# Kernel tuning notes

Measured on AMD Instinct MI355X. Metric: run time of the kernel, lower is better.

Reference implementation:

```python
import jax, jax.numpy as jnp
import numpy as np

N = 150000      # active voxels
C = 64          # head input channels
KK = 9          # 3x3 kernel offsets
H = W = 700     # BEV feature map
BN_EPS = 1e-5
HEADS = [("heatmap", 3), ("center", 2), ("center_z", 1), ("dim", 3), ("rot", 2)]


def _build_neighbor_table(seed=0):
    """Submanifold 3x3 neighbor indices for N active voxels on an HxW grid.
    Entry -1 means the neighbor site is inactive (contributes zero)."""
    rng = np.random.default_rng(seed)
    flat = rng.choice(H * W, size=N, replace=False)
    ys, xs = flat // W, flat % W
    lut = np.full(H * W, -1, np.int64)
    lut[flat] = np.arange(N)
    nbr = np.full((N, KK), -1, np.int64)
    k = 0
    for dy in (-1, 0, 1):
        for dx in (-1, 0, 1):
            ny, nx = ys + dy, xs + dx
            valid = (ny >= 0) & (ny < H) & (nx >= 0) & (nx < W)
            nf = np.where(valid, ny * W + nx, 0)
            nbr[:, k] = np.where(valid, lut[nf], -1)
            k += 1
    return nbr


def setup_inputs() -> dict:
    key = jax.random.key(0)
    ks = jax.random.split(key, 2 + 2 * len(HEADS))
    inp = {
        "features": jax.random.normal(ks[0], (N, C), jnp.float32),
        "nbr_idx": jnp.asarray(_build_neighbor_table(), jnp.int32),
        # one 3x3 subm conv per head, stacked: [n_heads, 9, C_in, C_out]
        "W3": jax.random.normal(ks[1], (len(HEADS), KK, C, C), jnp.float32) * 0.05,
        "gamma": jnp.ones((len(HEADS), C), jnp.float32),
        "beta": jnp.zeros((len(HEADS), C), jnp.float32),
    }
    for i, (name, oc) in enumerate(HEADS):
        inp[f"W1_{name}"] = jax.random.normal(ks[2 + i], (C, oc), jnp.float32) * 0.001
        if name == "heatmap":
            inp[f"b1_{name}"] = jnp.full((oc,), -float(np.log((1 - 0.01) / 0.01)), jnp.float32)
        else:
            inp[f"b1_{name}"] = jnp.zeros((oc,), jnp.float32)
    return inp


def _forward(features, nbr_idx, W3, gamma, beta, W1s, b1s):
    valid = nbr_idx >= 0                                  # [N, 9]
    idx = jnp.where(valid, nbr_idx, 0)
    # gather active-neighbor features; missing neighbors -> zero (subm conv)
    gathered = features[idx] * valid[..., None].astype(features.dtype)  # [N, 9, C]
    # all heads share the same input sparse tensor -> batched gather-GEMM
    h = jnp.einsum('nkc,hkco->hno', gathered, W3)         # [n_heads, N, C]
    # BatchNorm1d (training-mode batch stats, biased var) + ReLU
    mean = h.mean(axis=1, keepdims=True)
    var = ((h - mean) ** 2).mean(axis=1, keepdims=True)
    hn = (h - mean) * jax.lax.rsqrt(var + BN_EPS)
    hn = jax.nn.relu(hn * gamma[:, None, :] + beta[:, None, :])
    # per-head 1x1 subm conv == linear on active features
    return tuple(hn[i] @ W1s[i] + b1s[i] for i in range(len(HEADS)))


def reference(features, nbr_idx, W3, gamma, beta,
              W1_heatmap, b1_heatmap, W1_center, b1_center,
              W1_center_z, b1_center_z, W1_dim, b1_dim, W1_rot, b1_rot):
    W1s = [W1_heatmap, W1_center, W1_center_z, W1_dim, W1_rot]
    b1s = [b1_heatmap, b1_center, b1_center_z, b1_dim, b1_rot]
    return _forward(features, nbr_idx, W3, gamma, beta, W1s, b1s)
```

## Files before the change

kernel.cpp:

```cpp
#include <hip/hip_runtime.h>

#define NVOX 150000
#define BM 128
#define MTILES 1172
#define SROW 150016
#define NCOL 320

typedef __attribute__((ext_vector_type(8))) short bf16x8;
typedef __attribute__((ext_vector_type(4))) float f32x4;

__device__ __forceinline__ unsigned short f2bf(float f) {
    unsigned u = __builtin_bit_cast(unsigned, f);
    u += 0x7fffu + ((u >> 16) & 1u);
    return (unsigned short)(u >> 16);
}

__device__ __forceinline__ void gld16(const void* g, void* l) {
    __builtin_amdgcn_global_load_lds(
        (const __attribute__((address_space(1))) unsigned int*)g,
        (__attribute__((address_space(3))) unsigned int*)l, 16, 0, 0);
}

__global__ void prep_feat(const float* __restrict__ src, unsigned short* __restrict__ dst) {
    int i = blockIdx.x * 256 + threadIdx.x;
    if (i < NVOX * 64) dst[i] = f2bf(src[i]);
    else if (i < NVOX * 64 + 64) dst[i] = 0;
}

__global__ void prep_w3(const float* __restrict__ w3, unsigned short* __restrict__ bt,
                        float* __restrict__ stats) {
    int i = blockIdx.x * 256 + threadIdx.x;
    int h = i / 36864;
    int rem = i - h * 36864;
    int kk = rem >> 12;
    int c = (rem >> 6) & 63;
    int o = rem & 63;
    bt[(size_t)(((h * 9 + kk) * 8) + (c >> 3)) * 512 + o * 8 + (c & 7)] = f2bf(w3[i]);
    if (i < 2 * NCOL) stats[i] = 0.f;
}

__global__ __launch_bounds__(256, 4)
void gemm_kernel(const unsigned short* __restrict__ featB,
                 const unsigned short* __restrict__ Bt2,
                 const int* __restrict__ nbr,
                 unsigned short* __restrict__ hbuf,
                 float* __restrict__ stats) {
    __shared__ __align__(16) char smem[30208];
    constexpr int SB_OFF = 16384;
    constexpr int IDX_OFF = 24576;
    constexpr int SRED_OFF = 29184;

    int bid = blockIdx.x;
    int r = bid & 7, q = bid >> 3;
    int ntile = q % 5;
    int mtile = (q / 5) * 8 + r;
    if (mtile >= MTILES) return;
    int m0 = mtile * BM;
    int n0 = ntile * 64;

    int tid = threadIdx.x;
    int w = tid >> 6, lane = tid & 63;
    int quad = lane >> 4, m16 = lane & 15;

    for (int lin = tid; lin < BM * 9; lin += 256) {
        int row = lin / 9, kkq = lin - row * 9;
        int v = -1;
        if (m0 + row < NVOX) v = nbr[(size_t)(m0 + row) * 9 + kkq];
        *(int*)(smem + IDX_OFF + (kkq * BM + row) * 4) = ((v < 0) ? NVOX : v) * 128;
    }
    __syncthreads();

    f32x4 acc[4][2];
#pragma unroll
    for (int mt = 0; mt < 4; ++mt)
#pragma unroll
        for (int nt = 0; nt < 2; ++nt)
            acc[mt][nt] = (f32x4){0.f, 0.f, 0.f, 0.f};

    const char* fb = (const char*)featB;
    const char* bsrc = (const char*)Bt2 + (size_t)ntile * 73728;
    char* sA = smem;
    char* sB = smem + SB_OFF;

    int mrow = (w >> 1) * 64;
    int ncol = (w & 1) * 32;

    for (int kk = 0; kk < 9; ++kk) {
        int off0 = *(const int*)(smem + IDX_OFF + (kk * BM + lane) * 4);
        int off1 = *(const int*)(smem + IDX_OFF + (kk * BM + 64 + lane) * 4);
        int c16a = w * 2, c16b = w * 2 + 1;
        gld16(fb + off0 + c16a * 16, sA + c16a * 2048);
        gld16(fb + off1 + c16a * 16, sA + c16a * 2048 + 1024);
        gld16(fb + off0 + c16b * 16, sA + c16b * 2048);
        gld16(fb + off1 + c16b * 16, sA + c16b * 2048 + 1024);
        gld16(bsrc + (kk * 8 + c16a) * 1024 + lane * 16, sB + c16a * 1024);
        gld16(bsrc + (kk * 8 + c16b) * 1024 + lane * 16, sB + c16b * 1024);
        __syncthreads();
        bf16x8 af[2][4], bfr[2][2];
#pragma unroll
        for (int ks = 0; ks < 2; ++ks) {
#pragma unroll
            for (int mt = 0; mt < 4; ++mt)
                af[ks][mt] = *(const bf16x8*)(sA + (ks * 4 + quad) * 2048 +
                                              (mrow + mt * 16 + m16) * 16);
#pragma unroll
            for (int nt = 0; nt < 2; ++nt)
                bfr[ks][nt] = *(const bf16x8*)(sB + (ks * 4 + quad) * 1024 +
                                               (ncol + nt * 16 + m16) * 16);
        }
#pragma unroll
        for (int ks = 0; ks < 2; ++ks)
#pragma unroll
            for (int mt = 0; mt < 4; ++mt)
#pragma unroll
                for (int nt = 0; nt < 2; ++nt)
                    acc[mt][nt] = __builtin_amdgcn_mfma_f32_16x16x32_bf16(
                        af[ks][mt], bfr[ks][nt], acc[mt][nt], 0, 0, 0);
        __syncthreads();
    }

#pragma unroll
    for (int mt = 0; mt < 4; ++mt) {
#pragma unroll
        for (int nt = 0; nt < 2; ++nt) {
            int col = ncol + nt * 16 + m16;
            int row = mrow + mt * 16 + quad * 4;
            f32x4 v = acc[mt][nt];
            unsigned lo = (unsigned)f2bf(v.x) | ((unsigned)f2bf(v.y) << 16);
            unsigned hi = (unsigned)f2bf(v.z) | ((unsigned)f2bf(v.w) << 16);
            uint2 pk; pk.x = lo; pk.y = hi;
            *(uint2*)(smem + col * 272 + row * 2) = pk;
        }
    }
    __syncthreads();
#pragma unroll
    for (int it = 0; it < 8; ++it) {
        int col = it * 8 + (tid >> 5);
        int l32 = tid & 31;
        uint2 v = *(const uint2*)(smem + col * 272 + l32 * 8);
        *(uint2*)(hbuf + (size_t)(n0 + col) * SROW + m0 + l32 * 4) = v;
    }

    float s[2], ss[2];
#pragma unroll
    for (int nt = 0; nt < 2; ++nt) {
        float a = 0.f, b = 0.f;
#pragma unroll
        for (int mt = 0; mt < 4; ++mt) {
            f32x4 v = acc[mt][nt];
            a += v.x + v.y + v.z + v.w;
            b += v.x * v.x + v.y * v.y + v.z * v.z + v.w * v.w;
        }
        s[nt] = a; ss[nt] = b;
        s[nt] += __shfl_xor(s[nt], 16); s[nt] += __shfl_xor(s[nt], 32);
        ss[nt] += __shfl_xor(ss[nt], 16); ss[nt] += __shfl_xor(ss[nt], 32);
    }
    if (quad == 0) {
#pragma unroll
        for (int nt = 0; nt < 2; ++nt) {
            float* p = (float*)(smem + SRED_OFF + ((w * 2 + nt) * 16 + m16) * 8);
            p[0] = s[nt]; p[1] = ss[nt];
        }
    }
    __syncthreads();
    if (tid < 64) {
        int col = tid;
        int half = col >> 5, nt = (col >> 4) & 1, mc = col & 15;
        const float* p0 = (const float*)(smem + SRED_OFF + ((half * 2 + nt) * 16 + mc) * 8);
        const float* p1 = (const float*)(smem + SRED_OFF + (((2 + half) * 2 + nt) * 16 + mc) * 8);
        atomicAdd(&stats[n0 + col], p0[0] + p1[0]);
        atomicAdd(&stats[NCOL + n0 + col], p0[1] + p1[1]);
    }
}

__global__ void head_kernel(const unsigned short* __restrict__ hbuf,
                            const float* __restrict__ stats,
                            const float* __restrict__ gamma, const float* __restrict__ beta,
                            const float* __restrict__ W1_0, const float* __restrict__ W1_1,
                            const float* __restrict__ W1_2, const float* __restrict__ W1_3,
                            const float* __restrict__ W1_4,
                            const float* __restrict__ b1_0, const float* __restrict__ b1_1,
                            const float* __restrict__ b1_2, const float* __restrict__ b1_3,
                            const float* __restrict__ b1_4,
                            float* __restrict__ out) {
    __shared__ float sScale[NCOL], sShift[NCOL], sW1[NCOL * 3], sB1[16];
    int tid = threadIdx.x;
    for (int c = tid; c < NCOL; c += 256) {
        float mean = stats[c] * (1.f / (float)NVOX);
        float var = stats[NCOL + c] * (1.f / (float)NVOX) - mean * mean;
        float inv = rsqrtf(var + 1e-5f);
        float sc = inv * gamma[c];
        sScale[c] = sc;
        sShift[c] = beta[c] - mean * sc;
    }
    for (int i = tid; i < 192; i += 256) { int cc = i / 3, jj = i - cc * 3; sW1[0 * 192 + i] = W1_0[cc * 3 + jj]; }
    for (int i = tid; i < 192; i += 256) { int cc = i / 3, jj = i - cc * 3; sW1[1 * 192 + i] = (jj < 2) ? W1_1[cc * 2 + jj] : 0.f; }
    for (int i = tid; i < 192; i += 256) { int cc = i / 3, jj = i - cc * 3; sW1[2 * 192 + i] = (jj < 1) ? W1_2[cc] : 0.f; }
    for (int i = tid; i < 192; i += 256) { int cc = i / 3, jj = i - cc * 3; sW1[3 * 192 + i] = W1_3[cc * 3 + jj]; }
    for (int i = tid; i < 192; i += 256) { int cc = i / 3, jj = i - cc * 3; sW1[4 * 192 + i] = (jj < 2) ? W1_4[cc * 2 + jj] : 0.f; }
    if (tid == 0) {
        sB1[0] = b1_0[0]; sB1[1] = b1_0[1]; sB1[2] = b1_0[2];
        sB1[3] = b1_1[0]; sB1[4] = b1_1[1]; sB1[5] = 0.f;
        sB1[6] = b1_2[0]; sB1[7] = 0.f;    sB1[8] = 0.f;
        sB1[9] = b1_3[0]; sB1[10] = b1_3[1]; sB1[11] = b1_3[2];
        sB1[12] = b1_4[0]; sB1[13] = b1_4[1]; sB1[14] = 0.f;
    }
    __syncthreads();
    int n = 2 * (blockIdx.x * 256 + tid);
    if (n >= NVOX) return;
    const unsigned short* hp = hbuf + n;
#pragma unroll
    for (int h = 0; h < 5; ++h) {
        float x0 = sB1[h * 3 + 0], x1 = sB1[h * 3 + 1], x2 = sB1[h * 3 + 2];
        float y0 = x0, y1 = x1, y2 = x2;
#pragma unroll 8
        for (int cc = 0; cc < 64; ++cc) {
            int c = h * 64 + cc;
            unsigned raw = *(const unsigned*)(hp + (size_t)c * SROW);
            float v0 = __builtin_bit_cast(float, raw << 16);
            float v1 = __builtin_bit_cast(float, raw & 0xffff0000u);
            float sc = sScale[c], sh = sShift[c];
            v0 = fmaxf(v0 * sc + sh, 0.f);
            v1 = fmaxf(v1 * sc + sh, 0.f);
            float w0 = sW1[c * 3 + 0], w1 = sW1[c * 3 + 1], w2 = sW1[c * 3 + 2];
            x0 += v0 * w0; x1 += v0 * w1; x2 += v0 * w2;
            y0 += v1 * w0; y1 += v1 * w1; y2 += v1 * w2;
        }
        if (h == 0) {
            out[n * 3 + 0] = x0; out[n * 3 + 1] = x1; out[n * 3 + 2] = x2;
            out[(n + 1) * 3 + 0] = y0; out[(n + 1) * 3 + 1] = y1; out[(n + 1) * 3 + 2] = y2;
        } else if (h == 1) {
            out[450000 + n * 2 + 0] = x0; out[450000 + n * 2 + 1] = x1;
            out[450000 + (n + 1) * 2 + 0] = y0; out[450000 + (n + 1) * 2 + 1] = y1;
        } else if (h == 2) {
            out[750000 + n] = x0; out[750000 + n + 1] = y0;
        } else if (h == 3) {
            out[900000 + n * 3 + 0] = x0; out[900000 + n * 3 + 1] = x1; out[900000 + n * 3 + 2] = x2;
            out[900000 + (n + 1) * 3 + 0] = y0; out[900000 + (n + 1) * 3 + 1] = y1; out[900000 + (n + 1) * 3 + 2] = y2;
        } else {
            out[1350000 + n * 2 + 0] = x0; out[1350000 + n * 2 + 1] = x1;
            out[1350000 + (n + 1) * 2 + 0] = y0; out[1350000 + (n + 1) * 2 + 1] = y1;
        }
    }
}

extern "C" void kernel_launch(void* const* d_in, const int* in_sizes, int n_in,
                              void* d_out, int out_size, void* d_ws, size_t ws_size,
                              hipStream_t stream) {
    const float* features = (const float*)d_in[0];
    const int* nbr        = (const int*)d_in[1];
    const float* w3       = (const float*)d_in[2];
    const float* gamma    = (const float*)d_in[3];
    const float* beta     = (const float*)d_in[4];
    const float* W1_0 = (const float*)d_in[5];  const float* b1_0 = (const float*)d_in[6];
    const float* W1_1 = (const float*)d_in[7];  const float* b1_1 = (const float*)d_in[8];
    const float* W1_2 = (const float*)d_in[9];  const float* b1_2 = (const float*)d_in[10];
    const float* W1_3 = (const float*)d_in[11]; const float* b1_3 = (const float*)d_in[12];
    const float* W1_4 = (const float*)d_in[13]; const float* b1_4 = (const float*)d_in[14];
    float* out = (float*)d_out;

    char* ws = (char*)d_ws;
    unsigned short* featB = (unsigned short*)ws;
    unsigned short* Bt2   = (unsigned short*)(ws + 19200128);
    float* stats          = (float*)(ws + 19568768);
    unsigned short* hbuf  = (unsigned short*)(ws + 19571328);

    prep_feat<<<(NVOX * 64 + 64 + 255) / 256, 256, 0, stream>>>(features, featB);
    prep_w3<<<184320 / 256, 256, 0, stream>>>(w3, Bt2, stats);
    gemm_kernel<<<8 * 5 * 147, 256, 0, stream>>>(featB, Bt2, nbr, hbuf, stats);
    head_kernel<<<(NVOX / 2 + 255) / 256, 256, 0, stream>>>(hbuf, stats, gamma, beta,
        W1_0, W1_1, W1_2, W1_3, W1_4, b1_0, b1_1, b1_2, b1_3, b1_4, out);
}
```

Baseline: 230.6 us.

## Enlarge GEMM M-tile, load weights to registers, vectorize prep, split head by head

The gather-GEMM tile grows to 256 rows, with each wave computing 64 rows by all 64 columns. Weight fragments now load straight from global into registers from a new row-major Bt layout instead of being staged through LDS, and occupancy bounds drop to 3 waves per SIMD. prep_feat now converts four floats per thread, and head_kernel spreads the five heads across separate threads for more parallelism. Together these aim to reuse each gathered A tile across more columns and to cut per-element overhead, at the cost of higher register pressure and more LDS per block.

```diff
diff --git a/kernel.cpp b/kernel.cpp
--- a/kernel.cpp
+++ b/kernel.cpp
@@ -1,13 +1,14 @@
 #include <hip/hip_runtime.h>
 
 #define NVOX 150000
-#define BM 128
-#define MTILES 1172
+#define BM 256
+#define MTILES 586
 #define SROW 150016
 #define NCOL 320
 
 typedef __attribute__((ext_vector_type(8))) short bf16x8;
 typedef __attribute__((ext_vector_type(4))) float f32x4;
+typedef __attribute__((ext_vector_type(4))) unsigned short us4;
 
 __device__ __forceinline__ unsigned short f2bf(float f) {
     unsigned u = __builtin_bit_cast(unsigned, f);
@@ -23,8 +24,14 @@
 
 __global__ void prep_feat(const float* __restrict__ src, unsigned short* __restrict__ dst) {
     int i = blockIdx.x * 256 + threadIdx.x;
-    if (i < NVOX * 64) dst[i] = f2bf(src[i]);
-    else if (i < NVOX * 64 + 64) dst[i] = 0;
+    if (i < NVOX * 16) {
+        const float4 v = *(const float4*)(src + (size_t)i * 4);
+        us4 o; o.x = f2bf(v.x); o.y = f2bf(v.y); o.z = f2bf(v.z); o.w = f2bf(v.w);
+        *(us4*)(dst + (size_t)i * 4) = o;
+    } else if (i < NVOX * 16 + 16) {
+        us4 z; z.x = 0; z.y = 0; z.z = 0; z.w = 0;
+        *(us4*)(dst + (size_t)i * 4) = z;
+    }
 }
 
 __global__ void prep_w3(const float* __restrict__ w3, unsigned short* __restrict__ bt,
@@ -35,20 +42,19 @@
     int kk = rem >> 12;
     int c = (rem >> 6) & 63;
     int o = rem & 63;
-    bt[(size_t)(((h * 9 + kk) * 8) + (c >> 3)) * 512 + o * 8 + (c & 7)] = f2bf(w3[i]);
+    bt[(size_t)(h * 64 + o) * 576 + kk * 64 + c] = f2bf(w3[i]);
     if (i < 2 * NCOL) stats[i] = 0.f;
 }
 
-__global__ __launch_bounds__(256, 4)
+__global__ __launch_bounds__(256, 3)
 void gemm_kernel(const unsigned short* __restrict__ featB,
-                 const unsigned short* __restrict__ Bt2,
+                 const unsigned short* __restrict__ Bt,
                  const int* __restrict__ nbr,
                  unsigned short* __restrict__ hbuf,
                  float* __restrict__ stats) {
-    __shared__ __align__(16) char smem[30208];
-    constexpr int SB_OFF = 16384;
-    constexpr int IDX_OFF = 24576;
-    constexpr int SRED_OFF = 29184;
+    __shared__ __align__(16) char smem[44032];
+    constexpr int IDX_OFF = 32768;
+    constexpr int SRED_OFF = 41984;
 
     int bid = blockIdx.x;
     int r = bid & 7, q = bid >> 3;
@@ -62,74 +68,77 @@
     int w = tid >> 6, lane = tid & 63;
     int quad = lane >> 4, m16 = lane & 15;
 
-    for (int lin = tid; lin < BM * 9; lin += 256) {
-        int row = lin / 9, kkq = lin - row * 9;
-        int v = -1;
-        if (m0 + row < NVOX) v = nbr[(size_t)(m0 + row) * 9 + kkq];
-        *(int*)(smem + IDX_OFF + (kkq * BM + row) * 4) = ((v < 0) ? NVOX : v) * 128;
-    }
-    __syncthreads();
-
-    f32x4 acc[4][2];
+    for (int lin = tid; lin < 2304; lin += 256) {
+        int kkq = lin >> 8, row = lin & 255;
+        int v = (m0 + row < NVOX) ? nbr[(size_t)(m0 + row) * 9 + kkq] : -1;
+        *(int*)(smem + IDX_OFF + lin * 4) = ((v < 0) ? NVOX : v) * 128;
+    }
+    __syncthreads();
+
+    f32x4 acc[4][4];
 #pragma unroll
     for (int mt = 0; mt < 4; ++mt)
 #pragma unroll
-        for (int nt = 0; nt < 2; ++nt)
+        for (int nt = 0; nt < 4; ++nt)
             acc[mt][nt] = (f32x4){0.f, 0.f, 0.f, 0.f};
 
     const char* fb = (const char*)featB;
-    const char* bsrc = (const char*)Bt2 + (size_t)ntile * 73728;
+    const unsigned short* bb[4];
+#pragma unroll
+    for (int nt = 0; nt < 4; ++nt)
+        bb[nt] = Bt + (size_t)(n0 + nt * 16 + m16) * 576 + quad * 8;
+
     char* sA = smem;
-    char* sB = smem + SB_OFF;
-
-    int mrow = (w >> 1) * 64;
-    int ncol = (w & 1) * 32;
 
     for (int kk = 0; kk < 9; ++kk) {
-        int off0 = *(const int*)(smem + IDX_OFF + (kk * BM + lane) * 4);
-        int off1 = *(const int*)(smem + IDX_OFF + (kk * BM + 64 + lane) * 4);
-        int c16a = w * 2, c16b = w * 2 + 1;
-        gld16(fb + off0 + c16a * 16, sA + c16a * 2048);
-        gld16(fb + off1 + c16a * 16, sA + c16a * 2048 + 1024);
-        gld16(fb + off0 + c16b * 16, sA + c16b * 2048);
-        gld16(fb + off1 + c16b * 16, sA + c16b * 2048 + 1024);
-        gld16(bsrc + (kk * 8 + c16a) * 1024 + lane * 16, sB + c16a * 1024);
-        gld16(bsrc + (kk * 8 + c16b) * 1024 + lane * 16, sB + c16b * 1024);
+        int off[4];
+#pragma unroll
+        for (int rg = 0; rg < 4; ++rg)
+            off[rg] = *(const int*)(smem + IDX_OFF + (kk * 256 + rg * 64 + lane) * 4);
+#pragma unroll
+        for (int cc = 0; cc < 2; ++cc) {
+            int c16 = w * 2 + cc;
+#pragma unroll
+            for (int rg = 0; rg < 4; ++rg)
+                gld16(fb + off[rg] + c16 * 16, sA + c16 * 4096 + rg * 1024 + lane * 16);
+        }
+        bf16x8 bfr[2][4];
+#pragma unroll
+        for (int ks = 0; ks < 2; ++ks)
+#pragma unroll
+            for (int nt = 0; nt < 4; ++nt)
+                bfr[ks][nt] = *(const bf16x8*)(bb[nt] + kk * 64 + ks * 32);
         __syncthreads();
-        bf16x8 af[2][4], bfr[2][2];
-#pragma unroll
-        for (int ks = 0; ks < 2; ++ks) {
+        bf16x8 af[2][4];
+#pragma unroll
+        for (int ks = 0; ks < 2; ++ks)
 #pragma unroll
             for (int mt = 0; mt < 4; ++mt)
-                af[ks][mt] = *(const bf16x8*)(sA + (ks * 4 + quad) * 2048 +
-                                              (mrow + mt * 16 + m16) * 16);
-#pragma unroll
-            for (int nt = 0; nt < 2; ++nt)
-                bfr[ks][nt] = *(const bf16x8*)(sB + (ks * 4 + quad) * 1024 +
-                                               (ncol + nt * 16 + m16) * 16);
-        }
+                af[ks][mt] = *(const bf16x8*)(sA + (ks * 4 + quad) * 4096 +
+                                              (w * 64 + mt * 16 + m16) * 16);
 #pragma unroll
         for (int ks = 0; ks < 2; ++ks)
 #pragma unroll
             for (int mt = 0; mt < 4; ++mt)
 #pragma unroll
-                for (int nt = 0; nt < 2; ++nt)
+                for (int nt = 0; nt < 4; ++nt)
                     acc[mt][nt] = __builtin_amdgcn_mfma_f32_16x16x32_bf16(
                         af[ks][mt], bfr[ks][nt], acc[mt][nt], 0, 0, 0);
         __syncthreads();
     }
 
+    unsigned short* sOut = (unsigned short*)smem;
 #pragma unroll
     for (int mt = 0; mt < 4; ++mt) {
 #pragma unroll
-        for (int nt = 0; nt < 2; ++nt) {
-            int col = ncol + nt * 16 + m16;
-            int row = mrow + mt * 16 + quad * 4;
+        for (int nt = 0; nt < 4; ++nt) {
+            int col = nt * 16 + m16;
+            int row = w * 64 + mt * 16 + quad * 4;
             f32x4 v = acc[mt][nt];
             unsigned lo = (unsigned)f2bf(v.x) | ((unsigned)f2bf(v.y) << 16);
             unsigned hi = (unsigned)f2bf(v.z) | ((unsigned)f2bf(v.w) << 16);
             uint2 pk; pk.x = lo; pk.y = hi;
-            *(uint2*)(smem + col * 272 + row * 2) = pk;
+            *(uint2*)(sOut + col * 264 + row) = pk;
         }
     }
     __syncthreads();
@@ -137,13 +146,13 @@
     for (int it = 0; it < 8; ++it) {
         int col = it * 8 + (tid >> 5);
         int l32 = tid & 31;
-        uint2 v = *(const uint2*)(smem + col * 272 + l32 * 8);
-        *(uint2*)(hbuf + (size_t)(n0 + col) * SROW + m0 + l32 * 4) = v;
-    }
-
-    float s[2], ss[2];
-#pragma unroll
-    for (int nt = 0; nt < 2; ++nt) {
+        uint4 v = *(const uint4*)(sOut + col * 264 + l32 * 8);
+        *(uint4*)(hbuf + (size_t)(n0 + col) * SROW + m0 + l32 * 8) = v;
+    }
+
+    float s[4], ss[4];
+#pragma unroll
+    for (int nt = 0; nt < 4; ++nt) {
         float a = 0.f, b = 0.f;
 #pragma unroll
         for (int mt = 0; mt < 4; ++mt) {
@@ -155,21 +164,25 @@
         s[nt] += __shfl_xor(s[nt], 16); s[nt] += __shfl_xor(s[nt], 32);
         ss[nt] += __shfl_xor(ss[nt], 16); ss[nt] += __shfl_xor(ss[nt], 32);
     }
+    float* sRed = (float*)(smem + SRED_OFF);
     if (quad == 0) {
 #pragma unroll
-        for (int nt = 0; nt < 2; ++nt) {
-            float* p = (float*)(smem + SRED_OFF + ((w * 2 + nt) * 16 + m16) * 8);
-            p[0] = s[nt]; p[1] = ss[nt];
+        for (int nt = 0; nt < 4; ++nt) {
+            sRed[((w * 4 + nt) * 16 + m16) * 2 + 0] = s[nt];
+            sRed[((w * 4 + nt) * 16 + m16) * 2 + 1] = ss[nt];
         }
     }
     __syncthreads();
     if (tid < 64) {
-        int col = tid;
-        int half = col >> 5, nt = (col >> 4) & 1, mc = col & 15;
-        const float* p0 = (const float*)(smem + SRED_OFF + ((half * 2 + nt) * 16 + mc) * 8);
-        const float* p1 = (const float*)(smem + SRED_OFF + (((2 + half) * 2 + nt) * 16 + mc) * 8);
-        atomicAdd(&stats[n0 + col], p0[0] + p1[0]);
-        atomicAdd(&stats[NCOL + n0 + col], p0[1] + p1[1]);
+        int nt = tid >> 4, c = tid & 15;
+        float a = 0.f, b = 0.f;
+#pragma unroll
+        for (int ww = 0; ww < 4; ++ww) {
+            a += sRed[((ww * 4 + nt) * 16 + c) * 2 + 0];
+            b += sRed[((ww * 4 + nt) * 16 + c) * 2 + 1];
+        }
+        atomicAdd(&stats[n0 + tid], a);
+        atomicAdd(&stats[NCOL + n0 + tid], b);
     }
 }
 
@@ -206,41 +219,42 @@
         sB1[12] = b1_4[0]; sB1[13] = b1_4[1]; sB1[14] = 0.f;
     }
     __syncthreads();
-    int n = 2 * (blockIdx.x * 256 + tid);
-    if (n >= NVOX) return;
+    int lin = blockIdx.x * 256 + tid;
+    int h = lin / 75008;
+    int rp = lin - h * 75008;
+    if (rp >= 75000) return;
+    int n = rp * 2;
     const unsigned short* hp = hbuf + n;
-#pragma unroll
-    for (int h = 0; h < 5; ++h) {
-        float x0 = sB1[h * 3 + 0], x1 = sB1[h * 3 + 1], x2 = sB1[h * 3 + 2];
-        float y0 = x0, y1 = x1, y2 = x2;
+    float x0 = sB1[h * 3 + 0], x1 = sB1[h * 3 + 1], x2 = sB1[h * 3 + 2];
+    float y0 = x0, y1 = x1, y2 = x2;
+    int cbase = h * 64;
 #pragma unroll 8
-        for (int cc = 0; cc < 64; ++cc) {
-            int c = h * 64 + cc;
-            unsigned raw = *(const unsigned*)(hp + (size_t)c * SROW);
-            float v0 = __builtin_bit_cast(float, raw << 16);
-            float v1 = __builtin_bit_cast(float, raw & 0xffff0000u);
-            float sc = sScale[c], sh = sShift[c];
-            v0 = fmaxf(v0 * sc + sh, 0.f);
-            v1 = fmaxf(v1 * sc + sh, 0.f);
-            float w0 = sW1[c * 3 + 0], w1 = sW1[c * 3 + 1], w2 = sW1[c * 3 + 2];
-            x0 += v0 * w0; x1 += v0 * w1; x2 += v0 * w2;
-            y0 += v1 * w0; y1 += v1 * w1; y2 += v1 * w2;
-        }
-        if (h == 0) {
-            out[n * 3 + 0] = x0; out[n * 3 + 1] = x1; out[n * 3 + 2] = x2;
-            out[(n + 1) * 3 + 0] = y0; out[(n + 1) * 3 + 1] = y1; out[(n + 1) * 3 + 2] = y2;
-        } else if (h == 1) {
-            out[450000 + n * 2 + 0] = x0; out[450000 + n * 2 + 1] = x1;
-            out[450000 + (n + 1) * 2 + 0] = y0; out[450000 + (n + 1) * 2 + 1] = y1;
-        } else if (h == 2) {
-            out[750000 + n] = x0; out[750000 + n + 1] = y0;
-        } else if (h == 3) {
-            out[900000 + n * 3 + 0] = x0; out[900000 + n * 3 + 1] = x1; out[900000 + n * 3 + 2] = x2;
-            out[900000 + (n + 1) * 3 + 0] = y0; out[900000 + (n + 1) * 3 + 1] = y1; out[900000 + (n + 1) * 3 + 2] = y2;
-        } else {
-            out[1350000 + n * 2 + 0] = x0; out[1350000 + n * 2 + 1] = x1;
-            out[1350000 + (n + 1) * 2 + 0] = y0; out[1350000 + (n + 1) * 2 + 1] = y1;
-        }
+    for (int cc = 0; cc < 64; ++cc) {
+        int c = cbase + cc;
+        unsigned raw = *(const unsigned*)(hp + (size_t)c * SROW);
+        float v0 = __builtin_bit_cast(float, raw << 16);
+        float v1 = __builtin_bit_cast(float, raw & 0xffff0000u);
+        float sc = sScale[c], sh = sShift[c];
+        v0 = fmaxf(v0 * sc + sh, 0.f);
+        v1 = fmaxf(v1 * sc + sh, 0.f);
+        float w0 = sW1[c * 3 + 0], w1 = sW1[c * 3 + 1], w2 = sW1[c * 3 + 2];
+        x0 += v0 * w0; x1 += v0 * w1; x2 += v0 * w2;
+        y0 += v1 * w0; y1 += v1 * w1; y2 += v1 * w2;
+    }
+    if (h == 0) {
+        out[n * 3 + 0] = x0; out[n * 3 + 1] = x1; out[n * 3 + 2] = x2;
+        out[(n + 1) * 3 + 0] = y0; out[(n + 1) * 3 + 1] = y1; out[(n + 1) * 3 + 2] = y2;
+    } else if (h == 1) {
+        out[450000 + n * 2 + 0] = x0; out[450000 + n * 2 + 1] = x1;
+        out[450000 + (n + 1) * 2 + 0] = y0; out[450000 + (n + 1) * 2 + 1] = y1;
+    } else if (h == 2) {
+        out[750000 + n] = x0; out[750000 + n + 1] = y0;
+    } else if (h == 3) {
+        out[900000 + n * 3 + 0] = x0; out[900000 + n * 3 + 1] = x1; out[900000 + n * 3 + 2] = x2;
+        out[900000 + (n + 1) * 3 + 0] = y0; out[900000 + (n + 1) * 3 + 1] = y1; out[900000 + (n + 1) * 3 + 2] = y2;
+    } else {
+        out[1350000 + n * 2 + 0] = x0; out[1350000 + n * 2 + 1] = x1;
+        out[1350000 + (n + 1) * 2 + 0] = y0; out[1350000 + (n + 1) * 2 + 1] = y1;
     }
 }
 
@@ -261,13 +275,13 @@
 
     char* ws = (char*)d_ws;
     unsigned short* featB = (unsigned short*)ws;
-    unsigned short* Bt2   = (unsigned short*)(ws + 19200128);
+    unsigned short* Bt    = (unsigned short*)(ws + 19200128);
     float* stats          = (float*)(ws + 19568768);
     unsigned short* hbuf  = (unsigned short*)(ws + 19571328);
 
-    prep_feat<<<(NVOX * 64 + 64 + 255) / 256, 256, 0, stream>>>(features, featB);
-    prep_w3<<<184320 / 256, 256, 0, stream>>>(w3, Bt2, stats);
-    gemm_kernel<<<8 * 5 * 147, 256, 0, stream>>>(featB, Bt2, nbr, hbuf, stats);
-    head_kernel<<<(NVOX / 2 + 255) / 256, 256, 0, stream>>>(hbuf, stats, gamma, beta,
+    prep_feat<<<(NVOX * 16 + 16 + 255) / 256, 256, 0, stream>>>(features, featB);
+    prep_w3<<<184320 / 256, 256, 0, stream>>>(w3, Bt, stats);
+    gemm_kernel<<<8 * 5 * 74, 256, 0, stream>>>(featB, Bt, nbr, hbuf, stats);
+    head_kernel<<<(5 * 75008) / 256, 256, 0, stream>>>(hbuf, stats, gamma, beta,
         W1_0, W1_1, W1_2, W1_3, W1_4, b1_0, b1_1, b1_2, b1_3, b1_4, out);
 }
```

New measurement: 300.0 us. 30.1% more time.

## Register-prefetch gathered rows with swizzled LDS, read weights from global, split head kernel by head

Applied to the files above, without the earlier changes.

The GEMM kernel drops the direct global-to-LDS loads. It now register-prefetches the next offset's gathered feature rows while computing the current one and stores them into an XOR-swizzled LDS tile. Weight fragments are read straight from a re-laid-out [head*64+o][kk*64+c] global array, which frees the B tile from LDS. The feature and weight prep kernels are vectorised and turned into a transpose through shared memory, and the head kernel gives each thread a single head to get five times more parallel threads. Together these aim to overlap gather latency with MFMA work and cut LDS traffic and occupancy pressure, at the cost of more registers and repeated global weight reads.

```diff
diff --git a/kernel.cpp b/kernel.cpp
--- a/kernel.cpp
+++ b/kernel.cpp
@@ -8,6 +8,7 @@
 
 typedef __attribute__((ext_vector_type(8))) short bf16x8;
 typedef __attribute__((ext_vector_type(4))) float f32x4;
+typedef __attribute__((ext_vector_type(4))) unsigned short us4;
 
 __device__ __forceinline__ unsigned short f2bf(float f) {
     unsigned u = __builtin_bit_cast(unsigned, f);
@@ -15,40 +16,54 @@
     return (unsigned short)(u >> 16);
 }
 
-__device__ __forceinline__ void gld16(const void* g, void* l) {
-    __builtin_amdgcn_global_load_lds(
-        (const __attribute__((address_space(1))) unsigned int*)g,
-        (__attribute__((address_space(3))) unsigned int*)l, 16, 0, 0);
-}
-
 __global__ void prep_feat(const float* __restrict__ src, unsigned short* __restrict__ dst) {
     int i = blockIdx.x * 256 + threadIdx.x;
-    if (i < NVOX * 64) dst[i] = f2bf(src[i]);
-    else if (i < NVOX * 64 + 64) dst[i] = 0;
+    if (i < NVOX * 8) {
+        const float4 a = *(const float4*)(src + (size_t)i * 8);
+        const float4 b = *(const float4*)(src + (size_t)i * 8 + 4);
+        us4 lo, hi;
+        lo.x = f2bf(a.x); lo.y = f2bf(a.y); lo.z = f2bf(a.z); lo.w = f2bf(a.w);
+        hi.x = f2bf(b.x); hi.y = f2bf(b.y); hi.z = f2bf(b.z); hi.w = f2bf(b.w);
+        *(us4*)(dst + (size_t)i * 8) = lo;
+        *(us4*)(dst + (size_t)i * 8 + 4) = hi;
+    } else if (i < NVOX * 8 + 8) {
+        us4 z; z.x = 0; z.y = 0; z.z = 0; z.w = 0;
+        *(us4*)(dst + (size_t)i * 8) = z;
+    }
 }
 
 __global__ void prep_w3(const float* __restrict__ w3, unsigned short* __restrict__ bt,
                         float* __restrict__ stats) {
-    int i = blockIdx.x * 256 + threadIdx.x;
-    int h = i / 36864;
-    int rem = i - h * 36864;
-    int kk = rem >> 12;
-    int c = (rem >> 6) & 63;
-    int o = rem & 63;
-    bt[(size_t)(((h * 9 + kk) * 8) + (c >> 3)) * 512 + o * 8 + (c & 7)] = f2bf(w3[i]);
-    if (i < 2 * NCOL) stats[i] = 0.f;
+    __shared__ float tile[64 * 65];
+    int b = blockIdx.x;
+    int tid = threadIdx.x;
+    const float* src = w3 + (size_t)b * 4096;
+#pragma unroll
+    for (int t = 0; t < 16; ++t) {
+        int lin = t * 256 + tid;
+        tile[(lin >> 6) * 65 + (lin & 63)] = src[lin];
+    }
+    __syncthreads();
+    int h = b / 9, kk = b - h * 9;
+    unsigned short* dst = bt + (size_t)h * 64 * 576 + kk * 64;
+#pragma unroll
+    for (int t = 0; t < 16; ++t) {
+        int lin = t * 256 + tid;
+        int o = lin >> 6, c = lin & 63;
+        dst[(size_t)o * 576 + c] = f2bf(tile[c * 65 + o]);
+    }
+    if (b == 0) for (int j = tid; j < 2 * NCOL; j += 256) stats[j] = 0.f;
 }
 
 __global__ __launch_bounds__(256, 4)
 void gemm_kernel(const unsigned short* __restrict__ featB,
-                 const unsigned short* __restrict__ Bt2,
+                 const unsigned short* __restrict__ Bt,
                  const int* __restrict__ nbr,
                  unsigned short* __restrict__ hbuf,
                  float* __restrict__ stats) {
-    __shared__ __align__(16) char smem[30208];
-    constexpr int SB_OFF = 16384;
-    constexpr int IDX_OFF = 24576;
-    constexpr int SRED_OFF = 29184;
+    __shared__ __align__(16) char smem[22016];
+    constexpr int IDX_OFF = 16384;
+    constexpr int SRED_OFF = 20992;
 
     int bid = blockIdx.x;
     int r = bid & 7, q = bid >> 3;
@@ -61,12 +76,13 @@
     int tid = threadIdx.x;
     int w = tid >> 6, lane = tid & 63;
     int quad = lane >> 4, m16 = lane & 15;
-
-    for (int lin = tid; lin < BM * 9; lin += 256) {
-        int row = lin / 9, kkq = lin - row * 9;
-        int v = -1;
-        if (m0 + row < NVOX) v = nbr[(size_t)(m0 + row) * 9 + kkq];
-        *(int*)(smem + IDX_OFF + (kkq * BM + row) * 4) = ((v < 0) ? NVOX : v) * 128;
+    int mrow = (w >> 1) * 64;
+    int ncol = (w & 1) * 32;
+
+    for (int lin = tid; lin < 1152; lin += 256) {
+        int kkq = lin >> 7, row = lin & 127;
+        int v = (m0 + row < NVOX) ? nbr[(size_t)(m0 + row) * 9 + kkq] : -1;
+        *(int*)(smem + IDX_OFF + lin * 4) = ((v < 0) ? NVOX : v) * 128;
     }
     __syncthreads();
 
@@ -78,47 +94,55 @@
             acc[mt][nt] = (f32x4){0.f, 0.f, 0.f, 0.f};
 
     const char* fb = (const char*)featB;
-    const char* bsrc = (const char*)Bt2 + (size_t)ntile * 73728;
     char* sA = smem;
-    char* sB = smem + SB_OFF;
-
-    int mrow = (w >> 1) * 64;
-    int ncol = (w & 1) * 32;
+    int srow_loc = tid >> 3;
+    int schunk = tid & 7;
+    int swz_base0 = (srow_loc * 128) + ((schunk ^ (srow_loc & 7)) * 16);
+
+    uint4 av[4];
+#pragma unroll
+    for (int i = 0; i < 4; ++i) {
+        int off = *(const int*)(smem + IDX_OFF + (0 * 128 + i * 32 + srow_loc) * 4);
+        av[i] = *(const uint4*)(fb + off + schunk * 16);
+    }
 
     for (int kk = 0; kk < 9; ++kk) {
-        int off0 = *(const int*)(smem + IDX_OFF + (kk * BM + lane) * 4);
-        int off1 = *(const int*)(smem + IDX_OFF + (kk * BM + 64 + lane) * 4);
-        int c16a = w * 2, c16b = w * 2 + 1;
-        gld16(fb + off0 + c16a * 16, sA + c16a * 2048);
-        gld16(fb + off1 + c16a * 16, sA + c16a * 2048 + 1024);
-        gld16(fb + off0 + c16b * 16, sA + c16b * 2048);
-        gld16(fb + off1 + c16b * 16, sA + c16b * 2048 + 1024);
-        gld16(bsrc + (kk * 8 + c16a) * 1024 + lane * 16, sB + c16a * 1024);
-        gld16(bsrc + (kk * 8 + c16b) * 1024 + lane * 16, sB + c16b * 1024);
         __syncthreads();
-        bf16x8 af[2][4], bfr[2][2];
+#pragma unroll
+        for (int i = 0; i < 4; ++i)
+            *(uint4*)(sA + i * 4096 + swz_base0) = av[i];
+        __syncthreads();
+        if (kk < 8) {
+#pragma unroll
+            for (int i = 0; i < 4; ++i) {
+                int off = *(const int*)(smem + IDX_OFF + ((kk + 1) * 128 + i * 32 + srow_loc) * 4);
+                av[i] = *(const uint4*)(fb + off + schunk * 16);
+            }
+        }
 #pragma unroll
         for (int ks = 0; ks < 2; ++ks) {
-#pragma unroll
-            for (int mt = 0; mt < 4; ++mt)
-                af[ks][mt] = *(const bf16x8*)(sA + (ks * 4 + quad) * 2048 +
-                                              (mrow + mt * 16 + m16) * 16);
+            bf16x8 af[4], bf[2];
+#pragma unroll
+            for (int mt = 0; mt < 4; ++mt) {
+                int row = mrow + mt * 16 + m16;
+                int chunk = (ks * 4 + quad) ^ (m16 & 7);
+                af[mt] = *(const bf16x8*)(sA + row * 128 + chunk * 16);
+            }
 #pragma unroll
             for (int nt = 0; nt < 2; ++nt)
-                bfr[ks][nt] = *(const bf16x8*)(sB + (ks * 4 + quad) * 1024 +
-                                               (ncol + nt * 16 + m16) * 16);
-        }
-#pragma unroll
-        for (int ks = 0; ks < 2; ++ks)
+                bf[nt] = *(const bf16x8*)(Bt + (size_t)(n0 + ncol + nt * 16 + m16) * 576 +
+                                          kk * 64 + ks * 32 + quad * 8);
 #pragma unroll
             for (int mt = 0; mt < 4; ++mt)
 #pragma unroll
                 for (int nt = 0; nt < 2; ++nt)
                     acc[mt][nt] = __builtin_amdgcn_mfma_f32_16x16x32_bf16(
-                        af[ks][mt], bfr[ks][nt], acc[mt][nt], 0, 0, 0);
-        __syncthreads();
-    }
-
+                        af[mt], bf[nt], acc[mt][nt], 0, 0, 0);
+        }
+    }
+
+    __syncthreads();
+    unsigned short* sOut = (unsigned short*)smem;
 #pragma unroll
     for (int mt = 0; mt < 4; ++mt) {
 #pragma unroll
@@ -129,7 +153,7 @@
             unsigned lo = (unsigned)f2bf(v.x) | ((unsigned)f2bf(v.y) << 16);
             unsigned hi = (unsigned)f2bf(v.z) | ((unsigned)f2bf(v.w) << 16);
             uint2 pk; pk.x = lo; pk.y = hi;
-            *(uint2*)(smem + col * 272 + row * 2) = pk;
+            *(uint2*)(sOut + col * 136 + row) = pk;
         }
     }
     __syncthreads();
@@ -137,7 +161,7 @@
     for (int it = 0; it < 8; ++it) {
         int col = it * 8 + (tid >> 5);
         int l32 = tid & 31;
-        uint2 v = *(const uint2*)(smem + col * 272 + l32 * 8);
+        uint2 v = *(const uint2*)(sOut + col * 136 + l32 * 4);
         *(uint2*)(hbuf + (size_t)(n0 + col) * SROW + m0 + l32 * 4) = v;
     }
 
@@ -155,19 +179,20 @@
         s[nt] += __shfl_xor(s[nt], 16); s[nt] += __shfl_xor(s[nt], 32);
         ss[nt] += __shfl_xor(ss[nt], 16); ss[nt] += __shfl_xor(ss[nt], 32);
     }
+    float* sRed = (float*)(smem + SRED_OFF);
     if (quad == 0) {
 #pragma unroll
         for (int nt = 0; nt < 2; ++nt) {
-            float* p = (float*)(smem + SRED_OFF + ((w * 2 + nt) * 16 + m16) * 8);
-            p[0] = s[nt]; p[1] = ss[nt];
+            sRed[((w * 2 + nt) * 16 + m16) * 2 + 0] = s[nt];
+            sRed[((w * 2 + nt) * 16 + m16) * 2 + 1] = ss[nt];
         }
     }
     __syncthreads();
     if (tid < 64) {
         int col = tid;
         int half = col >> 5, nt = (col >> 4) & 1, mc = col & 15;
-        const float* p0 = (const float*)(smem + SRED_OFF + ((half * 2 + nt) * 16 + mc) * 8);
-        const float* p1 = (const float*)(smem + SRED_OFF + (((2 + half) * 2 + nt) * 16 + mc) * 8);
+        const float* p0 = (const float*)(smem + SRED_OFF) + ((half * 2 + nt) * 16 + mc) * 2;
+        const float* p1 = (const float*)(smem + SRED_OFF) + (((2 + half) * 2 + nt) * 16 + mc) * 2;
         atomicAdd(&stats[n0 + col], p0[0] + p1[0]);
         atomicAdd(&stats[NCOL + n0 + col], p0[1] + p1[1]);
     }
@@ -206,41 +231,42 @@
         sB1[12] = b1_4[0]; sB1[13] = b1_4[1]; sB1[14] = 0.f;
     }
     __syncthreads();
-    int n = 2 * (blockIdx.x * 256 + tid);
-    if (n >= NVOX) return;
+    int lin = blockIdx.x * 256 + tid;
+    int h = lin / 75008;
+    int rp = lin - h * 75008;
+    if (rp >= 75000) return;
+    int n = rp * 2;
     const unsigned short* hp = hbuf + n;
-#pragma unroll
-    for (int h = 0; h < 5; ++h) {
-        float x0 = sB1[h * 3 + 0], x1 = sB1[h * 3 + 1], x2 = sB1[h * 3 + 2];
-        float y0 = x0, y1 = x1, y2 = x2;
+    float x0 = sB1[h * 3 + 0], x1 = sB1[h * 3 + 1], x2 = sB1[h * 3 + 2];
+    float y0 = x0, y1 = x1, y2 = x2;
+    int cbase = h * 64;
 #pragma unroll 8
-        for (int cc = 0; cc < 64; ++cc) {
-            int c = h * 64 + cc;
-            unsigned raw = *(const unsigned*)(hp + (size_t)c * SROW);
-            float v0 = __builtin_bit_cast(float, raw << 16);
-            float v1 = __builtin_bit_cast(float, raw & 0xffff0000u);
-            float sc = sScale[c], sh = sShift[c];
-            v0 = fmaxf(v0 * sc + sh, 0.f);
-            v1 = fmaxf(v1 * sc + sh, 0.f);
-            float w0 = sW1[c * 3 + 0], w1 = sW1[c * 3 + 1], w2 = sW1[c * 3 + 2];
-            x0 += v0 * w0; x1 += v0 * w1; x2 += v0 * w2;
-            y0 += v1 * w0; y1 += v1 * w1; y2 += v1 * w2;
-        }
-        if (h == 0) {
-            out[n * 3 + 0] = x0; out[n * 3 + 1] = x1; out[n * 3 + 2] = x2;
-            out[(n + 1) * 3 + 0] = y0; out[(n + 1) * 3 + 1] = y1; out[(n + 1) * 3 + 2] = y2;
-        } else if (h == 1) {
-            out[450000 + n * 2 + 0] = x0; out[450000 + n * 2 + 1] = x1;
-            out[450000 + (n + 1) * 2 + 0] = y0; out[450000 + (n + 1) * 2 + 1] = y1;
-        } else if (h == 2) {
-            out[750000 + n] = x0; out[750000 + n + 1] = y0;
-        } else if (h == 3) {
-            out[900000 + n * 3 + 0] = x0; out[900000 + n * 3 + 1] = x1; out[900000 + n * 3 + 2] = x2;
-            out[900000 + (n + 1) * 3 + 0] = y0; out[900000 + (n + 1) * 3 + 1] = y1; out[900000 + (n + 1) * 3 + 2] = y2;
-        } else {
-            out[1350000 + n * 2 + 0] = x0; out[1350000 + n * 2 + 1] = x1;
-            out[1350000 + (n + 1) * 2 + 0] = y0; out[1350000 + (n + 1) * 2 + 1] = y1;
-        }
+    for (int cc = 0; cc < 64; ++cc) {
+        int c = cbase + cc;
+        unsigned raw = *(const unsigned*)(hp + (size_t)c * SROW);
+        float v0 = __builtin_bit_cast(float, raw << 16);
+        float v1 = __builtin_bit_cast(float, raw & 0xffff0000u);
+        float sc = sScale[c], sh = sShift[c];
+        v0 = fmaxf(v0 * sc + sh, 0.f);
+        v1 = fmaxf(v1 * sc + sh, 0.f);
+        float w0 = sW1[c * 3 + 0], w1 = sW1[c * 3 + 1], w2 = sW1[c * 3 + 2];
+        x0 += v0 * w0; x1 += v0 * w1; x2 += v0 * w2;
+        y0 += v1 * w0; y1 += v1 * w1; y2 += v1 * w2;
+    }
+    if (h == 0) {
+        out[n * 3 + 0] = x0; out[n * 3 + 1] = x1; out[n * 3 + 2] = x2;
+        out[(n + 1) * 3 + 0] = y0; out[(n + 1) * 3 + 1] = y1; out[(n + 1) * 3 + 2] = y2;
+    } else if (h == 1) {
+        out[450000 + n * 2 + 0] = x0; out[450000 + n * 2 + 1] = x1;
+        out[450000 + (n + 1) * 2 + 0] = y0; out[450000 + (n + 1) * 2 + 1] = y1;
+    } else if (h == 2) {
+        out[750000 + n] = x0; out[750000 + n + 1] = y0;
+    } else if (h == 3) {
+        out[900000 + n * 3 + 0] = x0; out[900000 + n * 3 + 1] = x1; out[900000 + n * 3 + 2] = x2;
+        out[900000 + (n + 1) * 3 + 0] = y0; out[900000 + (n + 1) * 3 + 1] = y1; out[900000 + (n + 1) * 3 + 2] = y2;
+    } else {
+        out[1350000 + n * 2 + 0] = x0; out[1350000 + n * 2 + 1] = x1;
+        out[1350000 + (n + 1) * 2 + 0] = y0; out[1350000 + (n + 1) * 2 + 1] = y1;
     }
 }
 
@@ -261,13 +287,13 @@
 
     char* ws = (char*)d_ws;
     unsigned short* featB = (unsigned short*)ws;
-    unsigned short* Bt2   = (unsigned short*)(ws + 19200128);
+    unsigned short* Bt    = (unsigned short*)(ws + 19200128);
     float* stats          = (float*)(ws + 19568768);
     unsigned short* hbuf  = (unsigned short*)(ws + 19571328);
 
-    prep_feat<<<(NVOX * 64 + 64 + 255) / 256, 256, 0, stream>>>(features, featB);
-    prep_w3<<<184320 / 256, 256, 0, stream>>>(w3, Bt2, stats);
-    gemm_kernel<<<8 * 5 * 147, 256, 0, stream>>>(featB, Bt2, nbr, hbuf, stats);
-    head_kernel<<<(NVOX / 2 + 255) / 256, 256, 0, stream>>>(hbuf, stats, gamma, beta,
+    prep_feat<<<(NVOX * 8 + 8 + 255) / 256, 256, 0, stream>>>(features, featB);
+    prep_w3<<<45, 256, 0, stream>>>(w3, Bt, stats);
+    gemm_kernel<<<8 * 5 * 147, 256, 0, stream>>>(featB, Bt, nbr, hbuf, stats);
+    head_kernel<<<(5 * 75008) / 256, 256, 0, stream>>>(hbuf, stats, gamma, beta,
         W1_0, W1_1, W1_2, W1_3, W1_4, b1_0, b1_1, b1_2, b1_3, b1_4, out);
 }
```

New measurement: 413.6 us. +79.4%, slower.
